# Kernel optimization log

Hardware: AMD Instinct MI355X
Metric: run time of the kernel (lower is better)

Reference implementation:

```python
import jax, jax.numpy as jnp
import numpy as np

B, N, DK, DV = 16, 4096, 64, 64


def setup_inputs() -> dict:
    key = jax.random.key(0)
    kq, kk, kv = jax.random.split(key, 3)
    q = jax.random.normal(kq, (B, N, DK), dtype=jnp.float32)
    k = jax.random.normal(kk, (B, N, DK), dtype=jnp.float32)
    v = jax.random.normal(kv, (B, N, DV), dtype=jnp.float32)
    # causal mask: positions j<=i are attendable (mask==True)
    mask = jnp.tril(jnp.ones((N, N), dtype=bool))[None, :, :]  # (1, N, N)
    return {"q": q, "k": k, "v": v, "mask": mask}


def reference(q, k, v, mask):
    # scores: (B, N, N)
    scale = 1.0 / jnp.sqrt(jnp.asarray(q.shape[-1], dtype=q.dtype))
    scores = jnp.einsum('bnd,bmd->bnm', q, k) * scale
    scores = jnp.where(mask, scores, jnp.asarray(-jnp.inf, dtype=scores.dtype))
    attn = jax.nn.softmax(scores, axis=-1)
    # dropout is identity in eval/reference mode
    return jnp.einsum('bnm,bmd->bnd', attn, v)
```

## Files before the change

### kernel.cpp

```cpp
#include <hip/hip_runtime.h>


#define N_SEQ 4096
#define DIM   64
#define BM    64
#define BN    64

typedef __bf16  bf16x8 __attribute__((ext_vector_type(8)));
typedef unsigned short u16x8 __attribute__((ext_vector_type(8)));
typedef float   f32x4  __attribute__((ext_vector_type(4)));
typedef short   short4v __attribute__((ext_vector_type(4)));

static __device__ __forceinline__ unsigned short f2bf(float f) {
    unsigned int u = __float_as_uint(f);
    u += 0x7FFFu + ((u >> 16) & 1u);
    return (unsigned short)(u >> 16);
}

static __device__ __forceinline__ unsigned int pk2bf(float a, float b) {
#if defined(__HIP_DEVICE_COMPILE__) && __has_builtin(__builtin_amdgcn_cvt_pk_bf16_f32)
    typedef __bf16 bf16x2_t __attribute__((ext_vector_type(2)));
    bf16x2_t r = __builtin_amdgcn_cvt_pk_bf16_f32(a, b);
    return __builtin_bit_cast(unsigned int, r);
#else
    return (unsigned int)f2bf(a) | ((unsigned int)f2bf(b) << 16);
#endif
}

static __device__ __forceinline__ float fexp2(float x) {
#if defined(__HIP_DEVICE_COMPILE__) && __has_builtin(__builtin_amdgcn_exp2f)
    return __builtin_amdgcn_exp2f(x);
#else
    return exp2f(x);
#endif
}

static __device__ __forceinline__ bf16x8 ld_frag(const void* p) {
    u16x8 u = *reinterpret_cast<const u16x8*>(p);
    return __builtin_bit_cast(bf16x8, u);
}

static __device__ __forceinline__ f32x4 mfma_pv(uint2 a, uint2 b, f32x4 c) {
#if defined(__HIP_DEVICE_COMPILE__)
#if __has_builtin(__builtin_amdgcn_mfma_f32_16x16x16bf16_1k)
    return __builtin_amdgcn_mfma_f32_16x16x16bf16_1k(
        __builtin_bit_cast(short4v, a), __builtin_bit_cast(short4v, b), c, 0, 0, 0);
#else
    f32x4 d;
    asm volatile("v_mfma_f32_16x16x16_bf16 %0, %1, %2, %3"
                 : "=v"(d) : "v"(a), "v"(b), "v"(c));
    return d;
#endif
#else
    (void)a; (void)b;
    return c;
#endif
}

static __device__ __forceinline__ void gl_lds16(const unsigned short* g, unsigned short* l) {
#if defined(__HIP_DEVICE_COMPILE__)
    __builtin_amdgcn_global_load_lds(
        (const __attribute__((address_space(1))) unsigned int*)(g),
        (__attribute__((address_space(3))) unsigned int*)(l), 16, 0, 0);
#else
    (void)g; (void)l;
#endif
}

__global__ __launch_bounds__(256)
void prep_k(const float* __restrict__ K, unsigned short* __restrict__ wsK) {
    const int b = blockIdx.y, t = blockIdx.x;
    const float* src = K + ((size_t)b * N_SEQ + t * 64) * DIM;
    unsigned short* dst = wsK + ((size_t)(b * 64 + t)) * 4096;
    #pragma unroll
    for (int ph = 0; ph < 2; ++ph) {
        const int gidx = threadIdx.x + ph * 256;
        const int r = gidx >> 3, g = gidx & 7;
        const float* p = src + r * DIM + g * 8;
        f32x4 f0 = *reinterpret_cast<const f32x4*>(p);
        f32x4 f1 = *reinterpret_cast<const f32x4*>(p + 4);
        uint4 w;
        w.x = pk2bf(f0[0], f0[1]); w.y = pk2bf(f0[2], f0[3]);
        w.z = pk2bf(f1[0], f1[1]); w.w = pk2bf(f1[2], f1[3]);
        *reinterpret_cast<uint4*>(&dst[(r * 8 + (g ^ (r & 7))) * 8]) = w;
    }
}

__global__ __launch_bounds__(256)
void prep_v(const float* __restrict__ V, unsigned short* __restrict__ wsV) {
    const int b = blockIdx.y, t = blockIdx.x;
    const int dv = threadIdx.x & 63;
    const int g0 = threadIdx.x >> 6;
    const float* src = V + ((size_t)b * N_SEQ + t * 64) * DIM + dv;
    unsigned short* dst = wsV + ((size_t)(b * 64 + t)) * 4096;
    #pragma unroll
    for (int ph = 0; ph < 2; ++ph) {
        const int g = g0 + ph * 4;
        float p[8];
        #pragma unroll
        for (int i = 0; i < 8; ++i)
            p[i] = src[(size_t)(g * 8 + i) * DIM];
        uint4 w;
        w.x = pk2bf(p[0], p[1]); w.y = pk2bf(p[2], p[3]);
        w.z = pk2bf(p[4], p[5]); w.w = pk2bf(p[6], p[7]);
        *reinterpret_cast<uint4*>(&dst[(dv * 8 + (g ^ (dv & 7))) * 8]) = w;
    }
}

__global__ __launch_bounds__(256)
void attn_fwd(const float* __restrict__ Q, const unsigned short* __restrict__ wsK,
              const unsigned short* __restrict__ wsV, float* __restrict__ O) {
    __shared__ unsigned short kbuf[2][4096];
    __shared__ unsigned short vbuf[2][4096];

    const int tid  = threadIdx.x;
    const int wave = tid >> 6;
    const int lane = tid & 63;
    const int quad = lane >> 4;
    const int ln   = lane & 15;
    const int ln7  = lane & 7;

    const int b    = blockIdx.y;
    const int i0   = ((int)gridDim.x - 1 - (int)blockIdx.x) * BM;
    const int tmax = i0 >> 6;

    const float QS = 0.125f * 1.44269504f;
    const int qrow = i0 + wave * 16 + ln;
    const float* qptr = Q + ((size_t)b * N_SEQ + qrow) * DIM;
    u16x8 qa[2];
    #pragma unroll
    for (int s = 0; s < 2; ++s) {
        const float* p = qptr + s * 32 + quad * 8;
        f32x4 f0 = *reinterpret_cast<const f32x4*>(p);
        f32x4 f1 = *reinterpret_cast<const f32x4*>(p + 4);
        #pragma unroll
        for (int j = 0; j < 4; ++j) {
            qa[s][j]     = f2bf(f0[j] * QS);
            qa[s][4 + j] = f2bf(f1[j] * QS);
        }
    }

    int kaddr[8];
    #pragma unroll
    for (int s = 0; s < 2; ++s)
        #pragma unroll
        for (int nt = 0; nt < 4; ++nt)
            kaddr[s * 4 + nt] = (nt * 16 + ln) * 128 + (((s * 4 + quad) ^ ln7) * 16);
    int vaddr[16];
    #pragma unroll
    for (int nt = 0; nt < 4; ++nt)
        #pragma unroll
        for (int dvt = 0; dvt < 4; ++dvt)
            vaddr[nt * 4 + dvt] = (dvt * 16 + ln) * 128
                                + (((nt * 2 + (quad >> 1)) ^ ln7) * 16) + (quad & 1) * 8;

    const unsigned short* kt_src = wsK + (size_t)b * 64 * 4096;
    const unsigned short* vt_src = wsV + (size_t)b * 64 * 4096;
    const int dma_off = wave * 1024 + lane * 8;

    auto dma = [&](int t, int bufi) {
        const unsigned short* ks = kt_src + (size_t)t * 4096 + dma_off;
        const unsigned short* vs = vt_src + (size_t)t * 4096 + dma_off;
        #pragma unroll
        for (int i = 0; i < 2; ++i) {
            gl_lds16(ks + i * 512, &kbuf[bufi][wave * 1024 + i * 512]);
            gl_lds16(vs + i * 512, &vbuf[bufi][wave * 1024 + i * 512]);
        }
    };

    f32x4 o_acc[4] = {};
    float lsum = 0.f;

    auto compute = [&](int t, const unsigned short* kb, const unsigned short* vb) {
        f32x4 st[4] = {};
        #pragma unroll
        for (int s = 0; s < 2; ++s) {
            bf16x8 qf = __builtin_bit_cast(bf16x8, qa[s]);
            #pragma unroll
            for (int nt = 0; nt < 4; ++nt) {
                bf16x8 kf = ld_frag((const char*)kb + kaddr[s * 4 + nt]);
                st[nt] = __builtin_amdgcn_mfma_f32_16x16x32_bf16(kf, qf, st[nt], 0, 0, 0);
            }
        }
        uint2 pk_d[4];
        if (t == tmax) {
            const int qloc = wave * 16 + ln;
            #pragma unroll
            for (int nt = 0; nt < 4; ++nt) {
                float p[4];
                #pragma unroll
                for (int r = 0; r < 4; ++r) {
                    const int kp = nt * 16 + quad * 4 + r;
                    const float x = (kp > qloc) ? -3.0e38f : st[nt][r];
                    p[r] = fexp2(x);
                    lsum += p[r];
                }
                pk_d[nt].x = pk2bf(p[0], p[1]);
                pk_d[nt].y = pk2bf(p[2], p[3]);
            }
        } else {
            #pragma unroll
            for (int nt = 0; nt < 4; ++nt) {
                float p[4];
                #pragma unroll
                for (int r = 0; r < 4; ++r) {
                    p[r] = fexp2(st[nt][r]);
                    lsum += p[r];
                }
                pk_d[nt].x = pk2bf(p[0], p[1]);
                pk_d[nt].y = pk2bf(p[2], p[3]);
            }
        }
        #pragma unroll
        for (int nt = 0; nt < 4; ++nt)
            #pragma unroll
            for (int dvt = 0; dvt < 4; ++dvt) {
                uint2 bv = *reinterpret_cast<const uint2*>((const char*)vb + vaddr[nt * 4 + dvt]);
                o_acc[dvt] = mfma_pv(pk_d[nt], bv, o_acc[dvt]);
            }
    };

    dma(0, 0);
    int t = 0;
    while (true) {
        __syncthreads();
        if (t < tmax) dma(t + 1, 1);
        compute(t, kbuf[0], vbuf[0]);
        if (t == tmax) break;
        ++t;
        __syncthreads();
        if (t < tmax) dma(t + 1, 0);
        compute(t, kbuf[1], vbuf[1]);
        if (t == tmax) break;
        ++t;
    }

    float s = lsum;
    s += __shfl_xor(s, 16, 64);
    s += __shfl_xor(s, 32, 64);
    float linv[4];
    #pragma unroll
    for (int r = 0; r < 4; ++r)
        linv[r] = 1.0f / __shfl(s, quad * 4 + r, 64);

    float* obase = O + ((size_t)b * N_SEQ + i0 + wave * 16) * DIM;
    #pragma unroll
    for (int r = 0; r < 4; ++r)
        #pragma unroll
        for (int dvt = 0; dvt < 4; ++dvt)
            obase[(quad * 4 + r) * DIM + dvt * 16 + ln] = o_acc[dvt][r] * linv[r];
}

extern "C" void kernel_launch(void* const* d_in, const int* in_sizes, int n_in,
                              void* d_out, int out_size, void* d_ws, size_t ws_size,
                              hipStream_t stream) {
    const float* q = (const float*)d_in[0];
    const float* k = (const float*)d_in[1];
    const float* v = (const float*)d_in[2];
    float* out = (float*)d_out;

    unsigned short* wsK = (unsigned short*)d_ws;
    unsigned short* wsV = wsK + (size_t)16 * 64 * 4096;

    dim3 blk(256);
    prep_k<<<dim3(64, 16), blk, 0, stream>>>(k, wsK);
    prep_v<<<dim3(64, 16), blk, 0, stream>>>(v, wsV);
    attn_fwd<<<dim3(64, 16), blk, 0, stream>>>(q, wsK, wsV, out);
}
```

Baseline: 234.2 us.

## Merge K/V prep kernels, balance causal tile scheduling, prefetch V fragments

```diff
diff --git a/kernel.cpp b/kernel.cpp
--- a/kernel.cpp
+++ b/kernel.cpp
@@ -3,8 +3,6 @@
 
 #define N_SEQ 4096
 #define DIM   64
-#define BM    64
-#define BN    64
 
 typedef __bf16  bf16x8 __attribute__((ext_vector_type(8)));
 typedef unsigned short u16x8 __attribute__((ext_vector_type(8)));
@@ -68,42 +66,41 @@
 }
 
 __global__ __launch_bounds__(256)
-void prep_k(const float* __restrict__ K, unsigned short* __restrict__ wsK) {
+void prep_kv(const float* __restrict__ K, const float* __restrict__ V,
+             unsigned short* __restrict__ wsK, unsigned short* __restrict__ wsV) {
     const int b = blockIdx.y, t = blockIdx.x;
-    const float* src = K + ((size_t)b * N_SEQ + t * 64) * DIM;
-    unsigned short* dst = wsK + ((size_t)(b * 64 + t)) * 4096;
-    #pragma unroll
-    for (int ph = 0; ph < 2; ++ph) {
-        const int gidx = threadIdx.x + ph * 256;
-        const int r = gidx >> 3, g = gidx & 7;
-        const float* p = src + r * DIM + g * 8;
-        f32x4 f0 = *reinterpret_cast<const f32x4*>(p);
-        f32x4 f1 = *reinterpret_cast<const f32x4*>(p + 4);
-        uint4 w;
-        w.x = pk2bf(f0[0], f0[1]); w.y = pk2bf(f0[2], f0[3]);
-        w.z = pk2bf(f1[0], f1[1]); w.w = pk2bf(f1[2], f1[3]);
-        *reinterpret_cast<uint4*>(&dst[(r * 8 + (g ^ (r & 7))) * 8]) = w;
-    }
-}
-
-__global__ __launch_bounds__(256)
-void prep_v(const float* __restrict__ V, unsigned short* __restrict__ wsV) {
-    const int b = blockIdx.y, t = blockIdx.x;
-    const int dv = threadIdx.x & 63;
-    const int g0 = threadIdx.x >> 6;
-    const float* src = V + ((size_t)b * N_SEQ + t * 64) * DIM + dv;
-    unsigned short* dst = wsV + ((size_t)(b * 64 + t)) * 4096;
-    #pragma unroll
-    for (int ph = 0; ph < 2; ++ph) {
-        const int g = g0 + ph * 4;
-        float p[8];
-        #pragma unroll
-        for (int i = 0; i < 8; ++i)
-            p[i] = src[(size_t)(g * 8 + i) * DIM];
-        uint4 w;
-        w.x = pk2bf(p[0], p[1]); w.y = pk2bf(p[2], p[3]);
-        w.z = pk2bf(p[4], p[5]); w.w = pk2bf(p[6], p[7]);
-        *reinterpret_cast<uint4*>(&dst[(dv * 8 + (g ^ (dv & 7))) * 8]) = w;
+    if (blockIdx.z == 0) {
+        const float* src = K + ((size_t)b * N_SEQ + t * 64) * DIM;
+        unsigned short* dst = wsK + ((size_t)(b * 64 + t)) * 4096;
+        #pragma unroll
+        for (int ph = 0; ph < 2; ++ph) {
+            const int gidx = threadIdx.x + ph * 256;
+            const int r = gidx >> 3, g = gidx & 7;
+            const float* p = src + r * DIM + g * 8;
+            f32x4 f0 = *reinterpret_cast<const f32x4*>(p);
+            f32x4 f1 = *reinterpret_cast<const f32x4*>(p + 4);
+            uint4 w;
+            w.x = pk2bf(f0[0], f0[1]); w.y = pk2bf(f0[2], f0[3]);
+            w.z = pk2bf(f1[0], f1[1]); w.w = pk2bf(f1[2], f1[3]);
+            *reinterpret_cast<uint4*>(&dst[(r * 8 + (g ^ (r & 7))) * 8]) = w;
+        }
+    } else {
+        const int dv = threadIdx.x & 63;
+        const int g0 = threadIdx.x >> 6;
+        const float* src = V + ((size_t)b * N_SEQ + t * 64) * DIM + dv;
+        unsigned short* dst = wsV + ((size_t)(b * 64 + t)) * 4096;
+        #pragma unroll
+        for (int ph = 0; ph < 2; ++ph) {
+            const int g = g0 + ph * 4;
+            float p[8];
+            #pragma unroll
+            for (int i = 0; i < 8; ++i)
+                p[i] = src[(size_t)(g * 8 + i) * DIM];
+            uint4 w;
+            w.x = pk2bf(p[0], p[1]); w.y = pk2bf(p[2], p[3]);
+            w.z = pk2bf(p[4], p[5]); w.w = pk2bf(p[6], p[7]);
+            *reinterpret_cast<uint4*>(&dst[(dv * 8 + (g ^ (dv & 7))) * 8]) = w;
+        }
     }
 }
 
@@ -120,9 +117,14 @@
     const int ln   = lane & 15;
     const int ln7  = lane & 7;
 
-    const int b    = blockIdx.y;
-    const int i0   = ((int)gridDim.x - 1 - (int)blockIdx.x) * BM;
-    const int tmax = i0 >> 6;
+    const int L = (int)blockIdx.x;
+    const int u = L & 255, v = L >> 8;
+    const int p_ = u + ((v >> 1) << 8);
+    const int b    = p_ >> 5;
+    const int j    = p_ & 31;
+    const int tile = (v & 1) ? (63 - j) : j;
+    const int i0   = tile * 64;
+    const int tmax = tile;
 
     const float QS = 0.125f * 1.44269504f;
     const int qrow = i0 + wave * 16 + ln;
@@ -134,9 +136,9 @@
         f32x4 f0 = *reinterpret_cast<const f32x4*>(p);
         f32x4 f1 = *reinterpret_cast<const f32x4*>(p + 4);
         #pragma unroll
-        for (int j = 0; j < 4; ++j) {
-            qa[s][j]     = f2bf(f0[j] * QS);
-            qa[s][4 + j] = f2bf(f1[j] * QS);
+        for (int jj = 0; jj < 4; ++jj) {
+            qa[s][jj]     = f2bf(f0[jj] * QS);
+            qa[s][4 + jj] = f2bf(f1[jj] * QS);
         }
     }
 
@@ -182,6 +184,11 @@
                 st[nt] = __builtin_amdgcn_mfma_f32_16x16x32_bf16(kf, qf, st[nt], 0, 0, 0);
             }
         }
+        uint2 bvv[16];
+        #pragma unroll
+        for (int i = 0; i < 16; ++i)
+            bvv[i] = *reinterpret_cast<const uint2*>((const char*)vb + vaddr[i]);
+
         uint2 pk_d[4];
         if (t == tmax) {
             const int qloc = wave * 16 + ln;
@@ -214,10 +221,8 @@
         #pragma unroll
         for (int nt = 0; nt < 4; ++nt)
             #pragma unroll
-            for (int dvt = 0; dvt < 4; ++dvt) {
-                uint2 bv = *reinterpret_cast<const uint2*>((const char*)vb + vaddr[nt * 4 + dvt]);
-                o_acc[dvt] = mfma_pv(pk_d[nt], bv, o_acc[dvt]);
-            }
+            for (int dvt = 0; dvt < 4; ++dvt)
+                o_acc[dvt] = mfma_pv(pk_d[nt], bvv[nt * 4 + dvt], o_acc[dvt]);
     };
 
     dma(0, 0);
@@ -262,8 +267,6 @@
     unsigned short* wsK = (unsigned short*)d_ws;
     unsigned short* wsV = wsK + (size_t)16 * 64 * 4096;
 
-    dim3 blk(256);
-    prep_k<<<dim3(64, 16), blk, 0, stream>>>(k, wsK);
-    prep_v<<<dim3(64, 16), blk, 0, stream>>>(v, wsV);
-    attn_fwd<<<dim3(64, 16), blk, 0, stream>>>(q, wsK, wsV, out);
-}
+    prep_kv<<<dim3(64, 16, 2), dim3(256), 0, stream>>>(k, v, wsK, wsV);
+    attn_fwd<<<dim3(1024), dim3(256), 0, stream>>>(q, wsK, wsV, out);
+}
```

Result: faster. 212.3 us (-9.4%).
